# Kernel optimization log

Hardware: AMD Instinct MI355X
Metric: run time of the kernel (lower is better)

## Reference

```python
import jax, jax.numpy as jnp
import numpy as np

N_NODES = 100000
N_EDGES = 1600000
F_IN, HID, N_CLS = 64, 64, 40


def setup_inputs() -> dict:
    key = jax.random.key(0)
    ks = jax.random.split(key, 8)
    feats = jax.random.normal(ks[0], (N_NODES, F_IN), dtype=jnp.float32)
    src = jax.random.randint(ks[1], (N_EDGES,), 0, N_NODES, dtype=jnp.int32)
    dst = jax.random.randint(ks[2], (N_EDGES,), 0, N_NODES, dtype=jnp.int32)
    def lin(k, out_d, in_d):
        s = 1.0 / np.sqrt(in_d)
        return jax.random.uniform(k, (out_d, in_d), jnp.float32, -s, s)
    return {
        "features": feats,
        "src": src,
        "dst": dst,
        "W0": lin(ks[3], HID, F_IN), "b0": jnp.zeros((HID,), jnp.float32),
        "W1": lin(ks[4], HID, HID), "b1": jnp.zeros((HID,), jnp.float32),
        "W2": lin(ks[5], N_CLS, HID), "b2": jnp.zeros((N_CLS,), jnp.float32),
    }


def reference(features, src, dst, W0, b0, W1, b1, W2, b2):
    n = features.shape[0]
    # in-degrees (gcn aggregator normalizes by deg + 1, counting self-loop)
    deg = jax.ops.segment_sum(jnp.ones_like(dst, dtype=features.dtype), dst,
                              num_segments=n)  # [N]
    inv = 1.0 / (deg + 1.0)  # [N]

    def sage_gcn(h, W, b, act):
        # gather src features, sum into dst: message passing
        neigh = jax.ops.segment_sum(h[src], dst, num_segments=n)  # [N, d]
        h_neigh = (neigh + h) * inv[:, None]
        out = h_neigh @ W.T + b
        return jax.nn.relu(out) if act else out

    h = sage_gcn(features, W0, b0, True)
    h = sage_gcn(h, W1, b1, True)   # dropout = identity in eval mode
    h = sage_gcn(h, W2, b2, False)
    return h
```

## Files before the change

### kernel.cpp

```cpp
#include <hip/hip_runtime.h>
#include <hip/hip_bf16.h>


#define N_FEAT 64
#define CAP 64
#define CAPB 8
#define BSH 9
#define BSZ 512
#define OVF_CAP 4096

__device__ __forceinline__ float rl(float v, int l) {
    return __int_as_float(__builtin_amdgcn_readlane(__float_as_int(v), l));
}

__device__ __forceinline__ void bin_body(const int* __restrict__ src,
                                         const int* __restrict__ dst,
                                         unsigned int* __restrict__ bins,
                                         unsigned char* __restrict__ cnt8,
                                         int* __restrict__ ovf, int* __restrict__ ovf_cnt,
                                         int n_edges, int nbk, int nblk, int bid) {
    __shared__ int lcnt[256];
    const int tid = threadIdx.x;
    lcnt[tid] = 0;
    __syncthreads();

    const int e = bid * 256 + tid;
    const bool valid = e < n_edges;
    int s = 0, d = 0;
    if (valid) { s = src[e]; d = dst[e]; }
    const int b = d >> BSH;
    const unsigned int pack = ((unsigned int)(d & (BSZ - 1)) << 17) | (unsigned int)s;

    if (valid) {
        int slot = atomicAdd(&lcnt[b], 1);
        if (slot < CAPB) {
            bins[((size_t)b * nblk + bid) * CAPB + slot] = pack;
        } else {
            int p = atomicAdd(ovf_cnt, 1);
            if (p < OVF_CAP) { ovf[2 * p] = s; ovf[2 * p + 1] = d; }
        }
    }
    __syncthreads();
    if (tid < nbk) {
        int c = lcnt[tid];
        cnt8[(size_t)tid * nblk + bid] = (unsigned char)((c < CAPB) ? c : CAPB);
    }
}

__device__ __forceinline__ void transform64_body(const float* __restrict__ h,
                                                 const float* __restrict__ W,
                                                 float* __restrict__ t, int n_nodes, int bid) {
    const int lane = threadIdx.x & 63;
    const int wave = (bid << 2) | (threadIdx.x >> 6);
    float4 wreg[16];
    const float4* W4 = (const float4*)(W + lane * N_FEAT);
#pragma unroll
    for (int k = 0; k < 16; ++k) wreg[k] = W4[k];
    const float* wf = (const float*)wreg;

    const int node0 = wave * 8;
    for (int k = 0; k < 8; ++k) {
        const int node = node0 + k;
        if (node >= n_nodes) return;
        const float hv = h[(size_t)node * N_FEAT + lane];
        float acc = 0.f;
#pragma unroll
        for (int f = 0; f < 64; ++f) acc = fmaf(rl(hv, f), wf[f], acc);
        t[(size_t)node * N_FEAT + lane] = acc;
    }
}

__device__ __forceinline__ void ell_init_body(int* __restrict__ ell,
                                              float* __restrict__ xz,
                                              int n_nodes, int bid, int nb) {
    const size_t total4 = (size_t)n_nodes * (CAP / 4);
    int4* e4 = (int4*)ell;
    const int4 sv = make_int4(n_nodes, n_nodes, n_nodes, n_nodes);
    for (size_t i = (size_t)bid * 256 + threadIdx.x; i < total4; i += (size_t)nb * 256)
        e4[i] = sv;
    if (bid == 0 && threadIdx.x < 64) xz[threadIdx.x] = 0.f;
}

__global__ __launch_bounds__(256) void prep(const int* __restrict__ src,
                                            const int* __restrict__ dst,
                                            unsigned int* __restrict__ bins,
                                            unsigned char* __restrict__ cnt8,
                                            int* __restrict__ ovf, int* __restrict__ ovf_cnt,
                                            int n_edges, int nbk, int nblk,
                                            const float* __restrict__ feats,
                                            const float* __restrict__ W0,
                                            float* __restrict__ t0, int n_nodes,
                                            int* __restrict__ ell,
                                            int PB, int TB, int IB) {
    const int b = (int)blockIdx.x;
    if (b < PB)
        bin_body(src, dst, bins, cnt8, ovf, ovf_cnt, n_edges, nbk, nblk, b);
    else if (b < PB + TB)
        transform64_body(feats, W0, t0, n_nodes, b - PB);
    else
        ell_init_body(ell, t0 + (size_t)n_nodes * N_FEAT, n_nodes, b - PB - TB, IB);
}

__global__ __launch_bounds__(1024) void fill_scan(const unsigned int* __restrict__ bins,
                                                  const unsigned char* __restrict__ cnt8,
                                                  const int* __restrict__ ovf,
                                                  const int* __restrict__ ovf_cnt,
                                                  int* __restrict__ deg,
                                                  int* __restrict__ ell,
                                                  int nblk, int n_nodes) {
    __shared__ int lcnt[BSZ];
    const int tid = threadIdx.x;
    const int b = (int)blockIdx.x;
    if (tid < BSZ) lcnt[tid] = 0;
    __syncthreads();

    const int base_node = b << BSH;
    const int4* b4 = (const int4*)bins;
    const unsigned char* cb = cnt8 + (size_t)b * nblk;

    for (int seg = tid; seg < nblk; seg += 1024) {
        const int n = cb[seg];
        if (n == 0) continue;
        const size_t ro = ((size_t)b * nblk + seg) * 2;
        int4 r0 = b4[ro];
        int4 r1 = (n > 4) ? b4[ro + 1] : make_int4(0, 0, 0, 0);
        unsigned int rec[8] = {(unsigned)r0.x, (unsigned)r0.y, (unsigned)r0.z, (unsigned)r0.w,
                               (unsigned)r1.x, (unsigned)r1.y, (unsigned)r1.z, (unsigned)r1.w};
#pragma unroll
        for (int r = 0; r < CAPB; ++r) {
            if (r < n) {
                const unsigned int v = rec[r];
                const int ld = (int)(v >> 17);
                const int sv = (int)(v & 0x1FFFFu);
                const int slot = atomicAdd(&lcnt[ld], 1);
                if (slot < CAP) {
                    const int dn = base_node + ld;
                    ell[(((size_t)(slot >> 5) * n_nodes + dn) << 5) + (slot & 31)] = sv;
                }
            }
        }
    }

    int oc = *ovf_cnt;
    oc = (oc < OVF_CAP) ? oc : OVF_CAP;
    for (int i = tid; i < oc; i += 1024) {
        const int sv = ovf[2 * i], d = ovf[2 * i + 1];
        if ((d >> BSH) == b) {
            const int slot = atomicAdd(&lcnt[d - base_node], 1);
            if (slot < CAP)
                ell[(((size_t)(slot >> 5) * n_nodes + d) << 5) + (slot & 31)] = sv;
        }
    }
    __syncthreads();
    if (tid < BSZ) {
        const int node = base_node + tid;
        if (node < n_nodes) deg[node] = lcnt[tid];
    }
}

template <int OUTW, int NPW>
__global__ __launch_bounds__(256, 4) void agg_t_k(const float* __restrict__ t,
                                                  const float* __restrict__ bias,
                                                  const float* __restrict__ Wn,
                                                  const int* __restrict__ deg,
                                                  const int* __restrict__ ell,
                                                  float* __restrict__ tn,
                                                  int n_nodes) {
    __shared__ float4 sW[64 * 17];
    if (blockIdx.x == 0 && threadIdx.x < OUTW)
        tn[(size_t)n_nodes * OUTW + threadIdx.x] = 0.f;
    {
        const float4* Wg = (const float4*)Wn;
        for (int i = threadIdx.x; i < OUTW * 16; i += 256)
            sW[(i >> 4) * 17 + (i & 15)] = Wg[i];
    }
    __syncthreads();

    const int lane = threadIdx.x & 63;
    const int w = threadIdx.x >> 6;
    const int wave = (blockIdx.x << 2) | w;
    const int g = lane >> 4;
    const int q = lane & 15;
    const float4* t4 = (const float4*)t;
    const float4* tq = t4 + q;
    const int4* ell4 = (const int4*)ell;
    const float4 bq = ((const float4*)bias)[q];
    const int wrow = (OUTW == 64) ? lane : ((lane < OUTW) ? lane : 0);
    const float4* wrow4 = sW + wrow * 17;
    const bool has_out = (OUTW == 64) || (lane < OUTW);

    const int node0 = wave * NPW;
    if (node0 >= n_nodes) return;
    const int gi = g * 2;

#define GATH8(V, I)                         \
    do {                                    \
        V[0] = tq[(size_t)(I)[0].x * 16];   \
        V[1] = tq[(size_t)(I)[0].y * 16];   \
        V[2] = tq[(size_t)(I)[0].z * 16];   \
        V[3] = tq[(size_t)(I)[0].w * 16];   \
        V[4] = tq[(size_t)(I)[1].x * 16];   \
        V[5] = tq[(size_t)(I)[1].y * 16];   \
        V[6] = tq[(size_t)(I)[1].z * 16];   \
        V[7] = tq[(size_t)(I)[1].w * 16];   \
    } while (0)

#define EPILOGUE_GEMM(R)                                  \
    float o0 = 0.f, o1 = 0.f;                             \
    _Pragma("unroll")                                     \
    for (int c = 0; c < 16; c += 2) {                     \
        float4 w0 = wrow4[c];                             \
        float4 w1 = wrow4[c + 1];                         \
        o0 = fmaf(rl((R).x, c), w0.x, o0);                \
        o0 = fmaf(rl((R).y, c), w0.y, o0);                \
        o0 = fmaf(rl((R).z, c), w0.z, o0);                \
        o0 = fmaf(rl((R).w, c), w0.w, o0);                \
        o1 = fmaf(rl((R).x, c + 1), w1.x, o1);            \
        o1 = fmaf(rl((R).y, c + 1), w1.y, o1);            \
        o1 = fmaf(rl((R).z, c + 1), w1.z, o1);            \
        o1 = fmaf(rl((R).w, c + 1), w1.w, o1);            \
    }

    if (node0 + NPW <= n_nodes) {
        int dgv[NPW];
#pragma unroll
        for (int k = 0; k < NPW; ++k) dgv[k] = deg[node0 + k];

        int4 ix[2][2];
        float4 vb[2][8];
        float4 selfb[2];
        ix[0][0] = ell4[(size_t)node0 * 8 + gi];
        ix[0][1] = ell4[(size_t)node0 * 8 + gi + 1];
        if (NPW > 1) {
            ix[1][0] = ell4[(size_t)(node0 + 1) * 8 + gi];
            ix[1][1] = ell4[(size_t)(node0 + 1) * 8 + gi + 1];
        }
        selfb[0] = t4[(size_t)node0 * 16 + q];
        GATH8(vb[0], ix[0]);

#pragma unroll
        for (int k = 0; k < NPW; ++k) {
            if (k + 1 < NPW) {
                selfb[(k + 1) & 1] = t4[(size_t)(node0 + k + 1) * 16 + q];
                GATH8(vb[(k + 1) & 1], ix[(k + 1) & 1]);
            }
            if (k + 2 < NPW) {
                ix[k & 1][0] = ell4[(size_t)(node0 + k + 2) * 8 + gi];
                ix[k & 1][1] = ell4[(size_t)(node0 + k + 2) * 8 + gi + 1];
            }
            const int node = node0 + k;
            const int d = dgv[k];
            const float4* v = vb[k & 1];
            float4 acc;
            acc.x = ((v[0].x + v[1].x) + (v[2].x + v[3].x)) +
                    ((v[4].x + v[5].x) + (v[6].x + v[7].x));
            acc.y = ((v[0].y + v[1].y) + (v[2].y + v[3].y)) +
                    ((v[4].y + v[5].y) + (v[6].y + v[7].y));
            acc.z = ((v[0].z + v[1].z) + (v[2].z + v[3].z)) +
                    ((v[4].z + v[5].z) + (v[6].z + v[7].z));
            acc.w = ((v[0].w + v[1].w) + (v[2].w + v[3].w)) +
                    ((v[4].w + v[5].w) + (v[6].w + v[7].w));

            if (d > 32) {
                int4 j0 = ell4[((size_t)(n_nodes + node)) * 8 + gi];
                int4 j1 = ell4[((size_t)(n_nodes + node)) * 8 + gi + 1];
                {
                    float4 u0 = tq[(size_t)j0.x * 16];
                    float4 u1 = tq[(size_t)j0.y * 16];
                    float4 u2 = tq[(size_t)j0.z * 16];
                    float4 u3 = tq[(size_t)j0.w * 16];
                    acc.x += (u0.x + u1.x) + (u2.x + u3.x);
                    acc.y += (u0.y + u1.y) + (u2.y + u3.y);
                    acc.z += (u0.z + u1.z) + (u2.z + u3.z);
                    acc.w += (u0.w + u1.w) + (u2.w + u3.w);
                }
                {
                    float4 u0 = tq[(size_t)j1.x * 16];
                    float4 u1 = tq[(size_t)j1.y * 16];
                    float4 u2 = tq[(size_t)j1.z * 16];
                    float4 u3 = tq[(size_t)j1.w * 16];
                    acc.x += (u0.x + u1.x) + (u2.x + u3.x);
                    acc.y += (u0.y + u1.y) + (u2.y + u3.y);
                    acc.z += (u0.z + u1.z) + (u2.z + u3.z);
                    acc.w += (u0.w + u1.w) + (u2.w + u3.w);
                }
            }

            acc.x += __shfl_xor(acc.x, 16, 64); acc.y += __shfl_xor(acc.y, 16, 64);
            acc.z += __shfl_xor(acc.z, 16, 64); acc.w += __shfl_xor(acc.w, 16, 64);
            acc.x += __shfl_xor(acc.x, 32, 64); acc.y += __shfl_xor(acc.y, 32, 64);
            acc.z += __shfl_xor(acc.z, 32, 64); acc.w += __shfl_xor(acc.w, 32, 64);

            const float invv = 1.0f / (float)(d + 1);
            float4 r;
            r.x = fmaxf((acc.x + selfb[k & 1].x) * invv + bq.x, 0.f);
            r.y = fmaxf((acc.y + selfb[k & 1].y) * invv + bq.y, 0.f);
            r.z = fmaxf((acc.z + selfb[k & 1].z) * invv + bq.z, 0.f);
            r.w = fmaxf((acc.w + selfb[k & 1].w) * invv + bq.w, 0.f);

            EPILOGUE_GEMM(r);
            if (has_out) tn[(size_t)node * OUTW + lane] = o0 + o1;
        }
    } else {
        for (int k = 0; k < NPW; ++k) {
            const int node = node0 + k;
            if (node >= n_nodes) return;
            const int d = deg[node];
            float4 acc = make_float4(0.f, 0.f, 0.f, 0.f);
            const int np = (d > 32) ? 2 : 1;
            for (int p = 0; p < np; ++p) {
                int4 ii[2];
                ii[0] = ell4[((size_t)p * n_nodes + node) * 8 + gi];
                ii[1] = ell4[((size_t)p * n_nodes + node) * 8 + gi + 1];
                float4 vv[8];
                GATH8(vv, ii);
                acc.x += ((vv[0].x + vv[1].x) + (vv[2].x + vv[3].x)) +
                         ((vv[4].x + vv[5].x) + (vv[6].x + vv[7].x));
                acc.y += ((vv[0].y + vv[1].y) + (vv[2].y + vv[3].y)) +
                         ((vv[4].y + vv[5].y) + (vv[6].y + vv[7].y));
                acc.z += ((vv[0].z + vv[1].z) + (vv[2].z + vv[3].z)) +
                         ((vv[4].z + vv[5].z) + (vv[6].z + vv[7].z));
                acc.w += ((vv[0].w + vv[1].w) + (vv[2].w + vv[3].w)) +
                         ((vv[4].w + vv[5].w) + (vv[6].w + vv[7].w));
            }
            acc.x += __shfl_xor(acc.x, 16, 64); acc.y += __shfl_xor(acc.y, 16, 64);
            acc.z += __shfl_xor(acc.z, 16, 64); acc.w += __shfl_xor(acc.w, 16, 64);
            acc.x += __shfl_xor(acc.x, 32, 64); acc.y += __shfl_xor(acc.y, 32, 64);
            acc.z += __shfl_xor(acc.z, 32, 64); acc.w += __shfl_xor(acc.w, 32, 64);
            float4 self = t4[(size_t)node * 16 + q];
            const float invv = 1.0f / (float)(d + 1);
            float4 r;
            r.x = fmaxf((acc.x + self.x) * invv + bq.x, 0.f);
            r.y = fmaxf((acc.y + self.y) * invv + bq.y, 0.f);
            r.z = fmaxf((acc.z + self.z) * invv + bq.z, 0.f);
            r.w = fmaxf((acc.w + self.w) * invv + bq.w, 0.f);
            EPILOGUE_GEMM(r);
            if (has_out) tn[(size_t)node * OUTW + lane] = o0 + o1;
        }
    }
#undef GATH8
#undef EPILOGUE_GEMM
}

template <int NPW>
__global__ __launch_bounds__(256) void agg40_k(const float* __restrict__ t,
                                               const float* __restrict__ bias,
                                               const int* __restrict__ deg,
                                               const int* __restrict__ ell,
                                               float* __restrict__ out, int n_nodes) {
    const int lane = threadIdx.x & 63;
    const int wave = (blockIdx.x << 2) | (threadIdx.x >> 6);
    const int g = lane / 10;
    const int q = lane - g * 10;
    const bool act = lane < 60;
    const float actf = act ? 1.f : 0.f;
    const float4* t4 = (const float4*)t;
    const float4 bq = ((const float4*)bias)[q];
    const int node0 = wave * NPW;
    if (node0 >= n_nodes) return;

    int nmax = NPW;
    if (node0 + NPW > n_nodes) nmax = n_nodes - node0;

    int dg[NPW];
#pragma unroll
    for (int k = 0; k < NPW; ++k) dg[k] = deg[node0 + ((k < nmax) ? k : 0)];

    auto eaddr = [&](int nd, int e) -> size_t {
        return (((size_t)(e >> 5) * n_nodes + nd) << 5) + (e & 31);
    };

    float4 vb[2][4];
    auto issue = [&](int slot, int k) {
        const int node = node0 + k;
        int i0 = ell[eaddr(node, g + 0)];
        int i1 = ell[eaddr(node, g + 6)];
        int i2 = ell[eaddr(node, g + 12)];
        int i3 = ell[eaddr(node, g + 18)];
        vb[slot][0] = t4[(size_t)i0 * 10 + q];
        vb[slot][1] = t4[(size_t)i1 * 10 + q];
        vb[slot][2] = t4[(size_t)i2 * 10 + q];
        vb[slot][3] = t4[(size_t)i3 * 10 + q];
    };

    issue(0, 0);
#pragma unroll
    for (int k = 0; k < NPW; ++k) {
        if (k + 1 < NPW) issue((k + 1) & 1, k + 1);
        if (k >= nmax) break;
        const int node = node0 + k;
        const int d = dg[k];
        const float4* v = vb[k & 1];
        float4 acc;
        acc.x = (v[0].x + v[1].x) + (v[2].x + v[3].x);
        acc.y = (v[0].y + v[1].y) + (v[2].y + v[3].y);
        acc.z = (v[0].z + v[1].z) + (v[2].z + v[3].z);
        acc.w = (v[0].w + v[1].w) + (v[2].w + v[3].w);

        const int dcap = (d < CAP) ? d : CAP;
        for (int u = 1; u * 24 < dcap; ++u) {
            const int eb = u * 24 + g;
            const bool k0 = act && (eb + 0 < d) && (eb + 0 < CAP);
            const bool k1 = act && (eb + 6 < d) && (eb + 6 < CAP);
            const bool k2 = act && (eb + 12 < d) && (eb + 12 < CAP);
            const bool k3 = act && (eb + 18 < d) && (eb + 18 < CAP);
            int i0 = k0 ? ell[eaddr(node, eb + 0)] : n_nodes;
            int i1 = k1 ? ell[eaddr(node, eb + 6)] : n_nodes;
            int i2 = k2 ? ell[eaddr(node, eb + 12)] : n_nodes;
            int i3 = k3 ? ell[eaddr(node, eb + 18)] : n_nodes;
            float4 w0 = t4[(size_t)i0 * 10 + q];
            float4 w1 = t4[(size_t)i1 * 10 + q];
            float4 w2 = t4[(size_t)i2 * 10 + q];
            float4 w3 = t4[(size_t)i3 * 10 + q];
            acc.x += (w0.x + w1.x) + (w2.x + w3.x);
            acc.y += (w0.y + w1.y) + (w2.y + w3.y);
            acc.z += (w0.z + w1.z) + (w2.z + w3.z);
            acc.w += (w0.w + w1.w) + (w2.w + w3.w);
        }

        acc.x *= actf; acc.y *= actf; acc.z *= actf; acc.w *= actf;
        acc.x += __shfl(acc.x, lane + 30, 64); acc.y += __shfl(acc.y, lane + 30, 64);
        acc.z += __shfl(acc.z, lane + 30, 64); acc.w += __shfl(acc.w, lane + 30, 64);
        float4 s1, s2;
        s1.x = __shfl(acc.x, lane + 10, 64); s2.x = __shfl(acc.x, lane + 20, 64);
        s1.y = __shfl(acc.y, lane + 10, 64); s2.y = __shfl(acc.y, lane + 20, 64);
        s1.z = __shfl(acc.z, lane + 10, 64); s2.z = __shfl(acc.z, lane + 20, 64);
        s1.w = __shfl(acc.w, lane + 10, 64); s2.w = __shfl(acc.w, lane + 20, 64);
        acc.x += s1.x + s2.x; acc.y += s1.y + s2.y;
        acc.z += s1.z + s2.z; acc.w += s1.w + s2.w;

        const float4 self = t4[(size_t)node * 10 + q];
        const float invv = 1.0f / (float)(d + 1);
        float4 r;
        r.x = (acc.x + self.x) * invv + bq.x;
        r.y = (acc.y + self.y) * invv + bq.y;
        r.z = (acc.z + self.z) * invv + bq.z;
        r.w = (acc.w + self.w) * invv + bq.w;
        if (lane < 10) ((float4*)out)[(size_t)node * 10 + q] = r;
    }
}

extern "C" void kernel_launch(void* const* d_in, const int* in_sizes, int n_in,
                              void* d_out, int out_size, void* d_ws, size_t ws_size,
                              hipStream_t stream) {
    const float* feats = (const float*)d_in[0];
    const int*   src   = (const int*)d_in[1];
    const int*   dst   = (const int*)d_in[2];
    const float* W0    = (const float*)d_in[3];
    const float* b0    = (const float*)d_in[4];
    const float* W1    = (const float*)d_in[5];
    const float* b1    = (const float*)d_in[6];
    const float* W2    = (const float*)d_in[7];
    const float* b2    = (const float*)d_in[8];
    float*       out   = (float*)d_out;

    const int N = in_sizes[0] / N_FEAT;
    const int E = in_sizes[1];
    const int NBLK = (E + 255) / 256;
    const int NBK = (N + BSZ - 1) >> BSH;

    char* p = (char*)d_ws;
    const size_t xb = ((size_t)N * N_FEAT + 64) * sizeof(float);
    float* X = (float*)p; p += xb;
    float* Y = (float*)p; p += xb;
    unsigned int* bins = (unsigned int*)Y;
    const size_t binsb = (size_t)NBK * NBLK * CAPB * sizeof(unsigned int);
    if (binsb > xb) p += binsb - xb;
    int* deg = (int*)p;     p += (size_t)N * sizeof(int);
    int* ovf_cnt = (int*)p; p += 16;
    int* ovf = (int*)p;     p += (size_t)OVF_CAP * 2 * sizeof(int);
    unsigned char* cnt8 = (unsigned char*)p;
    p += ((size_t)NBK * NBLK + 15) & ~(size_t)15;
    int* ell = (int*)p;     p += (size_t)N * CAP * sizeof(int);

    hipMemsetAsync(ovf_cnt, 0, sizeof(int), stream);

    constexpr int NPW = 4;
    const int PB = NBLK;
    const int TB = ((N + 7) / 8 + 3) / 4;
    const int IB = 1024;
    const int ab = ((N + NPW - 1) / NPW + 3) / 4;

    prep<<<PB + TB + IB, 256, 0, stream>>>(src, dst, bins, cnt8, ovf, ovf_cnt,
                                           E, NBK, NBLK, feats, W0, X, N, ell, PB, TB, IB);
    fill_scan<<<NBK, 1024, 0, stream>>>(bins, cnt8, ovf, ovf_cnt, deg, ell, NBLK, N);
    agg_t_k<64, NPW><<<ab, 256, 0, stream>>>(X, b0, W1, deg, ell, Y, N);
    agg_t_k<40, NPW><<<ab, 256, 0, stream>>>(Y, b1, W2, deg, ell, X, N);
    agg40_k<NPW><<<ab, 256, 0, stream>>>(X, b2, deg, ell, out, N);
}
```

Baseline: 339.3 us.

## Build ELL rows in shared memory and fold bin counts into records

Removes the separate 25.6MB ELL sentinel-fill pass: fill_scan now assembles the first 32 slots per node in LDS, prefilled with the sentinel, and writes them out with coalesced int4 stores. The second 32-slot half is initialised and written only for nodes with degree above 32. The per-bin count byte array is dropped and the count is packed into the upper bits of the first bin record. The bin layout is also transposed to bid-major and written with nontemporal stores. This adds a 64KB LDS footprint per fill_scan block, which limits occupancy, plus an LDS overflow buffer (OVL) that can silently drop edges if it overflows.

```diff
diff --git a/kernel.cpp b/kernel.cpp
--- a/kernel.cpp
+++ b/kernel.cpp
@@ -8,6 +8,7 @@
 #define BSH 9
 #define BSZ 512
 #define OVF_CAP 4096
+#define OVL 1024
 
 __device__ __forceinline__ float rl(float v, int l) {
     return __int_as_float(__builtin_amdgcn_readlane(__float_as_int(v), l));
@@ -16,10 +17,10 @@
 __device__ __forceinline__ void bin_body(const int* __restrict__ src,
                                          const int* __restrict__ dst,
                                          unsigned int* __restrict__ bins,
-                                         unsigned char* __restrict__ cnt8,
                                          int* __restrict__ ovf, int* __restrict__ ovf_cnt,
-                                         int n_edges, int nbk, int nblk, int bid) {
+                                         int n_edges, int nbk, int bid) {
     __shared__ int lcnt[256];
+    __shared__ unsigned int lrec0[256];
     const int tid = threadIdx.x;
     lcnt[tid] = 0;
     __syncthreads();
@@ -33,8 +34,10 @@
 
     if (valid) {
         int slot = atomicAdd(&lcnt[b], 1);
-        if (slot < CAPB) {
-            bins[((size_t)b * nblk + bid) * CAPB + slot] = pack;
+        if (slot == 0) {
+            lrec0[b] = pack;
+        } else if (slot < CAPB) {
+            __builtin_nontemporal_store(pack, &bins[((size_t)bid * nbk + b) * CAPB + slot]);
         } else {
             int p = atomicAdd(ovf_cnt, 1);
             if (p < OVF_CAP) { ovf[2 * p] = s; ovf[2 * p + 1] = d; }
@@ -43,7 +46,9 @@
     __syncthreads();
     if (tid < nbk) {
         int c = lcnt[tid];
-        cnt8[(size_t)tid * nblk + bid] = (unsigned char)((c < CAPB) ? c : CAPB);
+        c = (c < CAPB) ? c : CAPB;
+        const unsigned int v0 = (c == 0) ? 0u : (lrec0[tid] | ((unsigned int)c << 26));
+        __builtin_nontemporal_store(v0, &bins[((size_t)bid * nbk + tid) * CAPB]);
     }
 }
 
@@ -70,91 +75,119 @@
     }
 }
 
-__device__ __forceinline__ void ell_init_body(int* __restrict__ ell,
-                                              float* __restrict__ xz,
-                                              int n_nodes, int bid, int nb) {
-    const size_t total4 = (size_t)n_nodes * (CAP / 4);
-    int4* e4 = (int4*)ell;
-    const int4 sv = make_int4(n_nodes, n_nodes, n_nodes, n_nodes);
-    for (size_t i = (size_t)bid * 256 + threadIdx.x; i < total4; i += (size_t)nb * 256)
-        e4[i] = sv;
-    if (bid == 0 && threadIdx.x < 64) xz[threadIdx.x] = 0.f;
-}
-
 __global__ __launch_bounds__(256) void prep(const int* __restrict__ src,
                                             const int* __restrict__ dst,
                                             unsigned int* __restrict__ bins,
-                                            unsigned char* __restrict__ cnt8,
                                             int* __restrict__ ovf, int* __restrict__ ovf_cnt,
-                                            int n_edges, int nbk, int nblk,
+                                            int n_edges, int nbk,
                                             const float* __restrict__ feats,
                                             const float* __restrict__ W0,
-                                            float* __restrict__ t0, int n_nodes,
-                                            int* __restrict__ ell,
-                                            int PB, int TB, int IB) {
+                                            float* __restrict__ t0, int n_nodes, int PB) {
     const int b = (int)blockIdx.x;
     if (b < PB)
-        bin_body(src, dst, bins, cnt8, ovf, ovf_cnt, n_edges, nbk, nblk, b);
-    else if (b < PB + TB)
+        bin_body(src, dst, bins, ovf, ovf_cnt, n_edges, nbk, b);
+    else
         transform64_body(feats, W0, t0, n_nodes, b - PB);
-    else
-        ell_init_body(ell, t0 + (size_t)n_nodes * N_FEAT, n_nodes, b - PB - TB, IB);
 }
 
 __global__ __launch_bounds__(1024) void fill_scan(const unsigned int* __restrict__ bins,
-                                                  const unsigned char* __restrict__ cnt8,
                                                   const int* __restrict__ ovf,
                                                   const int* __restrict__ ovf_cnt,
                                                   int* __restrict__ deg,
                                                   int* __restrict__ ell,
-                                                  int nblk, int n_nodes) {
+                                                  float* __restrict__ xz,
+                                                  int nblk, int nbk, int n_nodes) {
+    __shared__ int lell[BSZ * 32];
     __shared__ int lcnt[BSZ];
+    __shared__ unsigned int lovf[OVL];
+    __shared__ int lovn;
     const int tid = threadIdx.x;
     const int b = (int)blockIdx.x;
+    const int base_node = b << BSH;
+
+    for (int i = tid; i < BSZ * 32; i += 1024) lell[i] = n_nodes;
     if (tid < BSZ) lcnt[tid] = 0;
+    if (tid == 0) lovn = 0;
+    if (b == 0 && tid < 64) xz[tid] = 0.f;
     __syncthreads();
 
-    const int base_node = b << BSH;
-    const int4* b4 = (const int4*)bins;
-    const unsigned char* cb = cnt8 + (size_t)b * nblk;
-
+    const uint4* b4 = (const uint4*)bins;
     for (int seg = tid; seg < nblk; seg += 1024) {
-        const int n = cb[seg];
+        const size_t ro = ((size_t)seg * nbk + b) * 2;
+        const uint4 r0 = b4[ro];
+        const int n = (int)(r0.x >> 26);
         if (n == 0) continue;
-        const size_t ro = ((size_t)b * nblk + seg) * 2;
-        int4 r0 = b4[ro];
-        int4 r1 = (n > 4) ? b4[ro + 1] : make_int4(0, 0, 0, 0);
-        unsigned int rec[8] = {(unsigned)r0.x, (unsigned)r0.y, (unsigned)r0.z, (unsigned)r0.w,
-                               (unsigned)r1.x, (unsigned)r1.y, (unsigned)r1.z, (unsigned)r1.w};
+        unsigned int rec[8];
+        rec[0] = r0.x & 0x03FFFFFFu; rec[1] = r0.y; rec[2] = r0.z; rec[3] = r0.w;
+        if (n > 4) {
+            const uint4 r1 = b4[ro + 1];
+            rec[4] = r1.x; rec[5] = r1.y; rec[6] = r1.z; rec[7] = r1.w;
+        }
 #pragma unroll
         for (int r = 0; r < CAPB; ++r) {
             if (r < n) {
                 const unsigned int v = rec[r];
-                const int ld = (int)(v >> 17);
+                const int ld = (int)((v >> 17) & (BSZ - 1));
                 const int sv = (int)(v & 0x1FFFFu);
                 const int slot = atomicAdd(&lcnt[ld], 1);
-                if (slot < CAP) {
-                    const int dn = base_node + ld;
-                    ell[(((size_t)(slot >> 5) * n_nodes + dn) << 5) + (slot & 31)] = sv;
+                if (slot < 32) {
+                    lell[(ld << 5) + slot] = sv;
+                } else if (slot < CAP) {
+                    int p = atomicAdd(&lovn, 1);
+                    if (p < OVL)
+                        lovf[p] = (unsigned)sv | ((unsigned)ld << 17) |
+                                  ((unsigned)(slot - 32) << 26);
                 }
             }
         }
     }
-
-    int oc = *ovf_cnt;
-    oc = (oc < OVF_CAP) ? oc : OVF_CAP;
-    for (int i = tid; i < oc; i += 1024) {
-        const int sv = ovf[2 * i], d = ovf[2 * i + 1];
-        if ((d >> BSH) == b) {
-            const int slot = atomicAdd(&lcnt[d - base_node], 1);
-            if (slot < CAP)
-                ell[(((size_t)(slot >> 5) * n_nodes + d) << 5) + (slot & 31)] = sv;
+    {
+        int oc = *ovf_cnt; oc = (oc < OVF_CAP) ? oc : OVF_CAP;
+        for (int i = tid; i < oc; i += 1024) {
+            const int d = ovf[2 * i + 1];
+            if ((d >> BSH) == b) {
+                const int sv = ovf[2 * i];
+                const int ld = d - base_node;
+                const int slot = atomicAdd(&lcnt[ld], 1);
+                if (slot < 32) {
+                    lell[(ld << 5) + slot] = sv;
+                } else if (slot < CAP) {
+                    int p = atomicAdd(&lovn, 1);
+                    if (p < OVL)
+                        lovf[p] = (unsigned)sv | ((unsigned)ld << 17) |
+                                  ((unsigned)(slot - 32) << 26);
+                }
+            }
         }
     }
     __syncthreads();
-    if (tid < BSZ) {
-        const int node = base_node + tid;
-        if (node < n_nodes) deg[node] = lcnt[tid];
+    for (int t = tid; t < BSZ; t += 1024) {
+        const int node = base_node + t;
+        if (node < n_nodes && lcnt[t] > 32) {
+            int* p1 = &ell[((size_t)(n_nodes + node)) << 5];
+            for (int j = 0; j < 32; ++j) p1[j] = n_nodes;
+        }
+    }
+    __syncthreads();
+    {
+        int nn = lovn; nn = (nn < OVL) ? nn : OVL;
+        for (int i = tid; i < nn; i += 1024) {
+            const unsigned int v = lovf[i];
+            const int sv = (int)(v & 0x1FFFFu);
+            const int ld = (int)((v >> 17) & (BSZ - 1));
+            const int sl = (int)(v >> 26);
+            ell[(((size_t)(n_nodes + base_node + ld)) << 5) + sl] = sv;
+        }
+    }
+    const int4* l4 = (const int4*)lell;
+    int4* e4 = (int4*)(ell + ((size_t)base_node << 5));
+    for (int i = tid; i < BSZ * 8; i += 1024) {
+        const int node = base_node + (i >> 3);
+        if (node < n_nodes) e4[i] = l4[i];
+    }
+    for (int t = tid; t < BSZ; t += 1024) {
+        const int node = base_node + t;
+        if (node < n_nodes) deg[node] = lcnt[t];
     }
 }
 
@@ -464,13 +497,11 @@
     float* X = (float*)p; p += xb;
     float* Y = (float*)p; p += xb;
     unsigned int* bins = (unsigned int*)Y;
-    const size_t binsb = (size_t)NBK * NBLK * CAPB * sizeof(unsigned int);
+    const size_t binsb = (size_t)NBLK * NBK * CAPB * sizeof(unsigned int);
     if (binsb > xb) p += binsb - xb;
     int* deg = (int*)p;     p += (size_t)N * sizeof(int);
     int* ovf_cnt = (int*)p; p += 16;
     int* ovf = (int*)p;     p += (size_t)OVF_CAP * 2 * sizeof(int);
-    unsigned char* cnt8 = (unsigned char*)p;
-    p += ((size_t)NBK * NBLK + 15) & ~(size_t)15;
     int* ell = (int*)p;     p += (size_t)N * CAP * sizeof(int);
 
     hipMemsetAsync(ovf_cnt, 0, sizeof(int), stream);
@@ -478,12 +509,12 @@
     constexpr int NPW = 4;
     const int PB = NBLK;
     const int TB = ((N + 7) / 8 + 3) / 4;
-    const int IB = 1024;
     const int ab = ((N + NPW - 1) / NPW + 3) / 4;
 
-    prep<<<PB + TB + IB, 256, 0, stream>>>(src, dst, bins, cnt8, ovf, ovf_cnt,
-                                           E, NBK, NBLK, feats, W0, X, N, ell, PB, TB, IB);
-    fill_scan<<<NBK, 1024, 0, stream>>>(bins, cnt8, ovf, ovf_cnt, deg, ell, NBLK, N);
+    prep<<<PB + TB, 256, 0, stream>>>(src, dst, bins, ovf, ovf_cnt,
+                                      E, NBK, feats, W0, X, N, PB);
+    fill_scan<<<NBK, 1024, 0, stream>>>(bins, ovf, ovf_cnt, deg, ell,
+                                        X + (size_t)N * N_FEAT, NBLK, NBK, N);
     agg_t_k<64, NPW><<<ab, 256, 0, stream>>>(X, b0, W1, deg, ell, Y, N);
     agg_t_k<40, NPW><<<ab, 256, 0, stream>>>(Y, b1, W2, deg, ell, X, N);
     agg40_k<NPW><<<ab, 256, 0, stream>>>(X, b2, deg, ell, out, N);
```

After: 345.4 us. Within noise of the previous version (+1.8%).
